# Optimization experiments

Measured on AMD Instinct MI355X. Metric: run time of the kernel, lower is better.

## Reference

```python
import jax, jax.numpy as jnp
import numpy as np

WIDTH = 2048
NUM_HEADS = 16
HEAD_DIM = WIDTH // NUM_HEADS  # 128
ROPE_DIMS = HEAD_DIM // 2      # 64, partial rotary
WINDOW = 512
ROPE_BASE = 10000.0
NEG_INF = -1e9


def apply_rope(x, dims, offset=0, base=ROPE_BASE):
    # x: [B, H, L, hd]; non-traditional (half-split) rotary on first `dims` dims.
    L = x.shape[2]
    half = dims // 2
    pos = (offset + jnp.arange(L)).astype(x.dtype)                     # [L]
    inv_freq = jnp.exp(-jnp.log(jnp.asarray(base, x.dtype)) * (jnp.arange(0, dims, 2).astype(x.dtype) / dims))  # [half]
    theta = pos[:, None] * inv_freq[None, :]                           # [L, half]
    cos = jnp.cos(theta)[None, None]                                   # [1,1,L,half]
    sin = jnp.sin(theta)[None, None]
    x1 = x[..., :half]
    x2 = x[..., half:dims]
    rest = x[..., dims:]
    rx1 = x1 * cos - x2 * sin
    rx2 = x1 * sin + x2 * cos
    return jnp.concatenate([rx1, rx2, rest], axis=-1)


def setup_inputs() -> dict:
    key = jax.random.key(0)
    ks = jax.random.split(key, 6)
    B, L, D, hd = 2, 2048, WIDTH, HEAD_DIM
    x = jax.random.normal(ks[0], (B, L, D), dtype=jnp.float32)
    Wq = jax.random.normal(ks[1], (D, D), dtype=jnp.float32) * 0.02
    Wk = jax.random.normal(ks[2], (D, hd), dtype=jnp.float32) * 0.02
    Wv = jax.random.normal(ks[3], (D, hd), dtype=jnp.float32) * 0.02
    Wo = jax.random.normal(ks[4], (D, D), dtype=jnp.float32) * 0.02
    bo = jax.random.normal(ks[5], (D,), dtype=jnp.float32) * 0.02
    return {"x": x, "Wq": Wq, "Wk": Wk, "Wv": Wv, "Wo": Wo, "bo": bo}


def reference(x, Wq, Wk, Wv, Wo, bo):
    B, L, D = x.shape
    H, hd = NUM_HEADS, HEAD_DIM
    scale = hd ** (-0.5)

    q = (x @ Wq).reshape(B, L, H, hd).transpose(0, 2, 1, 3)   # [B,H,L,hd]
    k = (x @ Wk).reshape(B, L, 1, hd).transpose(0, 2, 1, 3)   # [B,1,L,hd] (MQA)
    v = (x @ Wv).reshape(B, L, 1, hd).transpose(0, 2, 1, 3)

    q = apply_rope(q, ROPE_DIMS)
    k = apply_rope(k, ROPE_DIMS)

    # sliding-window causal mask: attend iff 0 <= i - j < WINDOW
    i = jnp.arange(L)[:, None]
    j = jnp.arange(L)[None, :]
    allowed = (i - j >= 0) & (i - j < WINDOW)                  # [L,L]
    mask = jnp.where(allowed, 0.0, NEG_INF).astype(x.dtype)

    scores = jnp.einsum("bhqd,bkd->bhqk", q, k[:, 0]) * scale  # [B,H,L,L]
    scores = scores + mask[None, None]
    attn = jax.nn.softmax(scores, axis=-1)
    out = jnp.einsum("bhqk,bkd->bhqd", attn, v[:, 0])          # [B,H,L,hd]
    out = out.transpose(0, 2, 1, 3).reshape(B, L, D)
    return out @ Wo + bo
```

## Files before the change

### kernel.cpp

```cpp
#include <hip/hip_runtime.h>
#include <hip/hip_bf16.h>
#include <stdint.h>


typedef float  f32x4  __attribute__((ext_vector_type(4)));
typedef __bf16 bf16x8 __attribute__((ext_vector_type(8)));

#define ASYNC_LD16(gp, lp)                                                     \
  __builtin_amdgcn_global_load_lds(                                            \
      (__attribute__((address_space(1))) void*)(gp),                           \
      (__attribute__((address_space(3))) void*)(lp), 16, 0, 0)

__global__ __launch_bounds__(256) void prep_all(
    const float* __restrict__ x, __hip_bfloat16* __restrict__ xb,
    const float* __restrict__ Wq, const float* __restrict__ Wk,
    const float* __restrict__ Wv, const float* __restrict__ Wo,
    __hip_bfloat16* __restrict__ wqkvT, __hip_bfloat16* __restrict__ woT) {
  __shared__ float t[32][33];
  int bid = blockIdx.x;
  if (bid < 8192) {
    const int i = bid * 256 + threadIdx.x;
    const float4 v = ((const float4*)x)[i];
    __align__(8) __hip_bfloat16 o[4] = {
        __float2bfloat16(v.x), __float2bfloat16(v.y),
        __float2bfloat16(v.z), __float2bfloat16(v.w)};
    *(uint2*)(xb + (size_t)i * 4) = *(uint2*)o;
    return;
  }
  bid -= 8192;
  const float* src;
  __hip_bfloat16* dst;
  int C, cb, rb;
  if (bid < 4096) {
    src = Wq; dst = wqkvT; C = 2048; cb = bid & 63; rb = bid >> 6;
  } else if (bid < 4352) {
    const int l = bid - 4096;
    src = Wk; dst = wqkvT + 2048ull * 2048; C = 128; cb = l & 3; rb = l >> 2;
  } else if (bid < 4608) {
    const int l = bid - 4352;
    src = Wv; dst = wqkvT + 2176ull * 2048; C = 128; cb = l & 3; rb = l >> 2;
  } else {
    const int l = bid - 4608;
    src = Wo; dst = woT; C = 2048; cb = l & 63; rb = l >> 6;
  }
  const int c0 = cb * 32, r0 = rb * 32;
  const int xx = threadIdx.x & 31, y = threadIdx.x >> 5;
#pragma unroll
  for (int i = 0; i < 32; i += 8)
    t[y + i][xx] = src[(size_t)(r0 + y + i) * C + c0 + xx];
  __syncthreads();
#pragma unroll
  for (int i = 0; i < 32; i += 8)
    dst[(size_t)(c0 + y + i) * 2048 + r0 + xx] = __float2bfloat16(t[xx][y + i]);
}

__device__ __forceinline__ void gemm_core64(const __bf16* __restrict__ A,
                                            const __bf16* __restrict__ BT,
                                            int K, __bf16* As, __bf16* Bs,
                                            f32x4 (&acc)[4][4]) {
  const int tid = threadIdx.x;
  const int wave = tid >> 6;
  const int lane = tid & 63;
  const int m0 = blockIdx.y * 128;
  const int n0 = blockIdx.x * 128;
  const int wm = (wave & 1) * 64;
  const int wn = (wave >> 1) * 64;
  const int ln = lane & 15;
  const int quad = lane >> 4;
  const int rdoff = (quad ^ ((ln >> 1) & 3)) * 8;

  size_t goff[4];
  int ldsoff[4];
#pragma unroll
  for (int i = 0; i < 4; i++) {
    const int cidx = (wave * 4 + i) * 64 + lane;
    const int p = cidx >> 9;
    const int pidx = cidx & 511;
    const int row = pidx >> 2;
    const int cc = pidx & 3;
    const int cg = cc ^ ((row >> 1) & 3);
    goff[i] = (size_t)row * K + p * 32 + cg * 8;
    ldsoff[i] = (wave * 4 + i) * 512;
  }
  const __bf16* Abase = A + (size_t)m0 * K;
  const __bf16* Bbase = BT + (size_t)n0 * K;

  for (int k0 = 0; k0 < K; k0 += 64) {
#pragma unroll
    for (int i = 0; i < 4; i++)
      ASYNC_LD16(Abase + k0 + goff[i], As + ldsoff[i]);
#pragma unroll
    for (int i = 0; i < 4; i++)
      ASYNC_LD16(Bbase + k0 + goff[i], Bs + ldsoff[i]);
    __syncthreads();
    bf16x8 af[4][2], bf[4][2];
#pragma unroll
    for (int i = 0; i < 4; i++)
#pragma unroll
      for (int p = 0; p < 2; p++)
        af[i][p] = *(const bf16x8*)&As[p * 4096 + (wm + i * 16 + ln) * 32 + rdoff];
#pragma unroll
    for (int j = 0; j < 4; j++)
#pragma unroll
      for (int p = 0; p < 2; p++)
        bf[j][p] = *(const bf16x8*)&Bs[p * 4096 + (wn + j * 16 + ln) * 32 + rdoff];
#pragma unroll
    for (int p = 0; p < 2; p++)
#pragma unroll
      for (int i = 0; i < 4; i++)
#pragma unroll
        for (int j = 0; j < 4; j++)
          acc[i][j] = __builtin_amdgcn_mfma_f32_16x16x32_bf16(af[i][p], bf[j][p],
                                                              acc[i][j], 0, 0, 0);
    __syncthreads();
  }
}

__global__ __launch_bounds__(256) void gemm_qkv(
    const __bf16* __restrict__ A, const __bf16* __restrict__ BT,
    __hip_bfloat16* __restrict__ qd, __hip_bfloat16* __restrict__ kd,
    __hip_bfloat16* __restrict__ vtd, int K) {
  __shared__ __align__(16) __bf16 As[128 * 64];
  __shared__ __align__(16) __bf16 Bs[128 * 64];
  f32x4 acc[4][4];
  const f32x4 zero = {0.f, 0.f, 0.f, 0.f};
#pragma unroll
  for (int i = 0; i < 4; i++)
#pragma unroll
    for (int j = 0; j < 4; j++) acc[i][j] = zero;
  gemm_core64(A, BT, K, As, Bs, acc);

  const int tid = threadIdx.x;
  const int wave = tid >> 6;
  const int lane = tid & 63;
  const int quad = lane >> 4;
  const int ln = lane & 15;
  const int m0 = blockIdx.y * 128;
  const int n0 = blockIdx.x * 128;
  const int wm = (wave & 1) * 64;
  const int wn = (wave >> 1) * 64;

  if (n0 == 2176) {
    const int bb = m0 >> 11;
    const int mloc = m0 & 2047;
#pragma unroll
    for (int i = 0; i < 4; i++) {
      const int rb = mloc + wm + i * 16 + quad * 4;
#pragma unroll
      for (int j = 0; j < 4; j++) {
        const int col = wn + j * 16 + ln;
        __align__(8) __hip_bfloat16 t4[4];
#pragma unroll
        for (int r = 0; r < 4; r++) t4[r] = __float2bfloat16(acc[i][j][r]);
        *(uint2*)(vtd + ((size_t)(bb * 128 + col)) * 2048 + rb) = *(uint2*)t4;
      }
    }
    return;
  }

  __hip_bfloat16* dst;
  int dstride, dcol;
  if (n0 < 2048) {
    dst = qd; dstride = 2048; dcol = n0;
  } else {
    dst = kd; dstride = 128; dcol = 0;
  }
  const bool dorope = (wn == 0);
  float invf0 = 0.f, invf1 = 0.f;
  if (dorope) {
    invf0 = expf(-0.28782313662425574f * (float)ln);
    invf1 = expf(-0.28782313662425574f * (float)(16 + ln));
  }

#pragma unroll
  for (int i = 0; i < 4; i++) {
#pragma unroll
    for (int r = 0; r < 4; r++) {
      const int row = m0 + wm + i * 16 + quad * 4 + r;
      float o0 = acc[i][0][r], o1 = acc[i][1][r];
      float o2 = acc[i][2][r], o3 = acc[i][3][r];
      if (dorope) {
        const float pos = (float)(row & 2047);
        float s0, c0, s1, c1;
        __sincosf(pos * invf0, &s0, &c0);
        __sincosf(pos * invf1, &s1, &c1);
        const float a0 = o0, b0 = o2, a1 = o1, b1 = o3;
        o0 = a0 * c0 - b0 * s0;
        o2 = a0 * s0 + b0 * c0;
        o1 = a1 * c1 - b1 * s1;
        o3 = a1 * s1 + b1 * c1;
      }
      __hip_bfloat16* rp = dst + (size_t)row * dstride + dcol + wn + ln;
      rp[0]  = __float2bfloat16(o0);
      rp[16] = __float2bfloat16(o1);
      rp[32] = __float2bfloat16(o2);
      rp[48] = __float2bfloat16(o3);
    }
  }
}

__global__ __launch_bounds__(256) void gemm_out(
    const __bf16* __restrict__ A, const __bf16* __restrict__ BT,
    float* __restrict__ C, const float* __restrict__ bias, int N, int K) {
  __shared__ __align__(16) __bf16 As[128 * 64];
  __shared__ __align__(16) __bf16 Bs[128 * 64];
  f32x4 acc[4][4];
  const f32x4 zero = {0.f, 0.f, 0.f, 0.f};
#pragma unroll
  for (int i = 0; i < 4; i++)
#pragma unroll
    for (int j = 0; j < 4; j++) acc[i][j] = zero;
  gemm_core64(A, BT, K, As, Bs, acc);

  const int tid = threadIdx.x;
  const int wave = tid >> 6;
  const int lane = tid & 63;
  const int m0 = blockIdx.y * 128;
  const int n0 = blockIdx.x * 128;
  const int wm = (wave & 1) * 64;
  const int wn = (wave >> 1) * 64;
  const int lrow = lane & 15;
#pragma unroll
  for (int j = 0; j < 4; j++) {
    const int col = n0 + wn + j * 16 + lrow;
    const float bv = bias[col];
#pragma unroll
    for (int i = 0; i < 4; i++) {
#pragma unroll
      for (int r = 0; r < 4; r++) {
        const int row = m0 + wm + i * 16 + (lane >> 4) * 4 + r;
        C[(size_t)row * N + col] = acc[i][j][r] + bv;
      }
    }
  }
}

__global__ __launch_bounds__(256) void attn_mfma(
    const __bf16* __restrict__ qb,
    const __bf16* __restrict__ kb,
    const __bf16* __restrict__ vtb,
    __hip_bfloat16* __restrict__ o)
{
  __shared__ __align__(16) __bf16 Ks[4][64 * 32];
  __shared__ __align__(16) __bf16 Vs[2][128 * 32];
  __shared__ __align__(16) __bf16 Ps[4][2][2][512];
  const int tid = threadIdx.x;
  const int wave = tid >> 6;
  const int lane = tid & 63;
  const int quad = lane >> 4;
  const int ln = lane & 15;
  const int bid = blockIdx.x;
  const int q0 = (bid & 15) * 128;
  const int h = (bid >> 4) & 15;
  const int b = bid >> 8;
  const int swr = (ln >> 1) & 3;
  const int rdoff = (quad ^ swr) * 8;

  bf16x8 qf[2][4];
#pragma unroll
  for (int g = 0; g < 2; g++) {
    const __bf16* qrow =
        qb + ((size_t)(b * 2048 + q0 + wave * 32 + g * 16 + ln)) * 2048 + h * 128;
#pragma unroll
    for (int ks = 0; ks < 4; ks++)
      qf[g][ks] = *(const bf16x8*)(qrow + ks * 32 + quad * 8);
  }

  f32x4 oacc[2][8];
  const f32x4 zero = {0.f, 0.f, 0.f, 0.f};
#pragma unroll
  for (int g = 0; g < 2; g++)
#pragma unroll
    for (int nb = 0; nb < 8; nb++) oacc[g][nb] = zero;
  float li[2][4] = {{0.f, 0.f, 0.f, 0.f}, {0.f, 0.f, 0.f, 0.f}};
  const float scale = 0.08838834764831845f;

  const __bf16* kbase = kb + (size_t)b * 2048 * 128;
  const __bf16* vbase = vtb + (size_t)b * 128 * 2048;

  const int tstart = (q0 >= 512) ? 0 : (512 - q0) / 64;
  for (int t = tstart; t < 10; ++t) {
    const int jt = q0 - 512 + 64 * t;
    __syncthreads();
    {
      const int key4 = lane >> 2, uu = lane & 3;
      const int sw = (key4 >> 1) & 3;
#pragma unroll
      for (int i = 0; i < 4; ++i) {
        const int c = wave * 4 + i;
        const int ks = c & 3, keybase = (c >> 2) * 16;
        ASYNC_LD16(kbase + (size_t)(jt + keybase + key4) * 128 + ks * 32 +
                       (uu ^ sw) * 8,
                   &Ks[ks][keybase * 32]);
      }
#pragma unroll
      for (int i = 0; i < 4; ++i) {
        const int c = wave * 4 + i;
        const int p = c & 1, dbase = (c >> 1) * 16;
        ASYNC_LD16(vbase + (size_t)(dbase + key4) * 2048 + jt + p * 32 +
                       (uu ^ sw) * 8,
                   &Vs[p][dbase * 32]);
      }
    }
    __syncthreads();

    f32x4 sacc[2][4];
#pragma unroll
    for (int g = 0; g < 2; g++)
#pragma unroll
      for (int j = 0; j < 4; j++) sacc[g][j] = zero;
#pragma unroll
    for (int j = 0; j < 4; j++)
#pragma unroll
      for (int ks = 0; ks < 4; ks++) {
        const bf16x8 kf = *(const bf16x8*)&Ks[ks][(j * 16 + ln) * 32 + rdoff];
#pragma unroll
        for (int g = 0; g < 2; g++)
          sacc[g][j] = __builtin_amdgcn_mfma_f32_16x16x32_bf16(qf[g][ks], kf,
                                                               sacc[g][j], 0, 0, 0);
      }

#pragma unroll
    for (int g = 0; g < 2; g++)
#pragma unroll
      for (int j = 0; j < 4; j++)
#pragma unroll
        for (int r = 0; r < 4; r++) {
          float v = sacc[g][j][r] * scale;
          const int d0 = (wave * 32 + g * 16 + quad * 4 + r) - (j * 16 + ln);
          if (t <= 1 && d0 >= (t << 6)) v = -1e30f;
          if (t >= 8 && d0 < ((t - 8) << 6)) v = -1e30f;
          v = fminf(v, 60.f);
          const float p = __expf(v);
          li[g][r] += p;
          const int ch = (j & 1) * 2 + (ln >> 3);
          const int swp = (quad * 2 + (r >> 1)) & 3;
          Ps[wave][g][j >> 1]
            [(quad * 4 + r) * 32 + (ch ^ swp) * 8 + (ln & 7)] = (__bf16)p;
        }

    const bf16x8 pf00 = *(const bf16x8*)&Ps[wave][0][0][ln * 32 + rdoff];
    const bf16x8 pf01 = *(const bf16x8*)&Ps[wave][0][1][ln * 32 + rdoff];
    const bf16x8 pf10 = *(const bf16x8*)&Ps[wave][1][0][ln * 32 + rdoff];
    const bf16x8 pf11 = *(const bf16x8*)&Ps[wave][1][1][ln * 32 + rdoff];
#pragma unroll
    for (int nb = 0; nb < 8; nb++) {
      const bf16x8 vf0 = *(const bf16x8*)&Vs[0][(nb * 16 + ln) * 32 + rdoff];
      const bf16x8 vf1 = *(const bf16x8*)&Vs[1][(nb * 16 + ln) * 32 + rdoff];
      oacc[0][nb] =
          __builtin_amdgcn_mfma_f32_16x16x32_bf16(pf00, vf0, oacc[0][nb], 0, 0, 0);
      oacc[0][nb] =
          __builtin_amdgcn_mfma_f32_16x16x32_bf16(pf01, vf1, oacc[0][nb], 0, 0, 0);
      oacc[1][nb] =
          __builtin_amdgcn_mfma_f32_16x16x32_bf16(pf10, vf0, oacc[1][nb], 0, 0, 0);
      oacc[1][nb] =
          __builtin_amdgcn_mfma_f32_16x16x32_bf16(pf11, vf1, oacc[1][nb], 0, 0, 0);
    }
  }

#pragma unroll
  for (int off = 1; off < 16; off <<= 1)
#pragma unroll
    for (int g = 0; g < 2; g++)
#pragma unroll
      for (int r = 0; r < 4; r++) li[g][r] += __shfl_xor(li[g][r], off);

#pragma unroll
  for (int g = 0; g < 2; g++) {
    __hip_bfloat16* obase =
        o + ((size_t)(b * 2048 + q0 + wave * 32 + g * 16 + quad * 4)) * 2048 +
        h * 128 + ln;
#pragma unroll
    for (int r = 0; r < 4; r++) {
      const float inv = 1.0f / li[g][r];
#pragma unroll
      for (int nb = 0; nb < 8; nb++)
        obase[(size_t)r * 2048 + nb * 16] = __float2bfloat16(oacc[g][nb][r] * inv);
    }
  }
}

extern "C" void kernel_launch(void* const* d_in, const int* in_sizes, int n_in,
                              void* d_out, int out_size, void* d_ws,
                              size_t ws_size, hipStream_t stream) {
  const float* x = (const float*)d_in[0];
  const float* Wq = (const float*)d_in[1];
  const float* Wk = (const float*)d_in[2];
  const float* Wv = (const float*)d_in[3];
  const float* Wo = (const float*)d_in[4];
  const float* bo = (const float*)d_in[5];
  float* out = (float*)d_out;

  char* w = (char*)d_ws;
  auto alloc = [&](size_t bytes) {
    void* p = (void*)w;
    w += (bytes + 255) & ~(size_t)255;
    return p;
  };
  __bf16* xb = (__bf16*)alloc(4096ull * 2048 * 2);
  __hip_bfloat16* wqkvT = (__hip_bfloat16*)alloc(2304ull * 2048 * 2);
  __hip_bfloat16* woT = (__hip_bfloat16*)alloc(2048ull * 2048 * 2);
  __hip_bfloat16* qbuf = (__hip_bfloat16*)alloc(4096ull * 2048 * 2);
  __hip_bfloat16* kbuf = (__hip_bfloat16*)alloc(4096ull * 128 * 2);
  __hip_bfloat16* vtb = (__hip_bfloat16*)alloc(4096ull * 128 * 2);
  __hip_bfloat16* attnb = (__hip_bfloat16*)xb;

  prep_all<<<16896, 256, 0, stream>>>(x, (__hip_bfloat16*)xb, Wq, Wk, Wv, Wo,
                                      wqkvT, woT);

  gemm_qkv<<<dim3(18, 32), 256, 0, stream>>>(xb, (const __bf16*)wqkvT, qbuf,
                                             kbuf, vtb, 2048);

  attn_mfma<<<512, 256, 0, stream>>>((const __bf16*)qbuf, (const __bf16*)kbuf,
                                     (const __bf16*)vtb, attnb);

  gemm_out<<<dim3(16, 32), 256, 0, stream>>>((const __bf16*)attnb,
                                             (const __bf16*)woT, out, bo, 2048,
                                             2048);
}
```

Measured before the change: 259.7 us.

## Double-buffer K/V tiles in attention and specialize mask modes via templates

The attention kernel now keeps two shared-memory K/V buffers. It issues the async global-to-LDS loads for the next tile before computing the current one, so each iteration needs one barrier instead of two and load latency can overlap MFMA work. The per-tile compute is moved into a templated helper, so the unmasked middle tiles skip the mask comparisons entirely. The cost is doubled LDS use for K/V, which may lower occupancy. The loop also relies on the trailing barrier and the async-load wait semantics being correct for the prefetched buffer.

Result: no change. 263.3 us (+1.4%).

```diff
diff --git a/kernel.cpp b/kernel.cpp
--- a/kernel.cpp
+++ b/kernel.cpp
@@ -235,15 +235,112 @@
   }
 }
 
+__device__ __forceinline__ void stage_kv(const __bf16* __restrict__ kbase,
+                                         const __bf16* __restrict__ vbase,
+                                         int jt, __bf16* Kb, __bf16* Vb,
+                                         int wave, int lane) {
+  const int key4 = lane >> 2, uu = lane & 3;
+  const int sw = (key4 >> 1) & 3;
+#pragma unroll
+  for (int i = 0; i < 4; ++i) {
+    const int c = wave * 4 + i;
+    const int ks = c & 3, keybase = (c >> 2) * 16;
+    ASYNC_LD16(kbase + (size_t)(jt + keybase + key4) * 128 + ks * 32 +
+                   (uu ^ sw) * 8,
+               Kb + ks * 2048 + keybase * 32);
+  }
+#pragma unroll
+  for (int i = 0; i < 4; ++i) {
+    const int c = wave * 4 + i;
+    const int p = c & 1, dbase = (c >> 1) * 16;
+    ASYNC_LD16(vbase + (size_t)(dbase + key4) * 2048 + jt + p * 32 +
+                   (uu ^ sw) * 8,
+               Vb + p * 4096 + dbase * 32);
+  }
+}
+
+template <int MODE>
+__device__ __forceinline__ void attn_tile(
+    const __bf16* __restrict__ Kb, const __bf16* __restrict__ Vb,
+    __bf16* __restrict__ PsW, const bf16x8 (&qf)[2][4], f32x4 (&oacc)[2][8],
+    float (&li)[2][4], int t, int wave, int quad, int ln, int rdoff) {
+  const f32x4 zero = {0.f, 0.f, 0.f, 0.f};
+  const float scale = 0.08838834764831845f;
+
+  f32x4 sacc[2][4];
+#pragma unroll
+  for (int g = 0; g < 2; g++)
+#pragma unroll
+    for (int j = 0; j < 4; j++) sacc[g][j] = zero;
+#pragma unroll
+  for (int j = 0; j < 4; j++)
+#pragma unroll
+    for (int ks = 0; ks < 4; ks++) {
+      const bf16x8 kf =
+          *(const bf16x8*)&Kb[ks * 2048 + (j * 16 + ln) * 32 + rdoff];
+#pragma unroll
+      for (int g = 0; g < 2; g++)
+        sacc[g][j] = __builtin_amdgcn_mfma_f32_16x16x32_bf16(qf[g][ks], kf,
+                                                             sacc[g][j], 0, 0, 0);
+    }
+
+#pragma unroll
+  for (int g = 0; g < 2; g++)
+#pragma unroll
+    for (int j = 0; j < 4; j++) {
+      const int ch = (j & 1) * 2 + (ln >> 3);
+#pragma unroll
+      for (int rp = 0; rp < 2; rp++) {
+        const int swp = (quad * 2 + rp) & 3;
+        __bf16* pw = PsW + (g * 2 + (j >> 1)) * 512 + (quad * 4 + rp * 2) * 32 +
+                     (ch ^ swp) * 8 + (ln & 7);
+#pragma unroll
+        for (int r2 = 0; r2 < 2; r2++) {
+          const int r = rp * 2 + r2;
+          float vv = sacc[g][j][r] * scale;
+          if (MODE == 1) {
+            const int d0 = (wave * 32 + g * 16 + quad * 4 + r) - (j * 16 + ln);
+            if (d0 >= (t << 6)) vv = -1e30f;
+          } else if (MODE == 2) {
+            const int d0 = (wave * 32 + g * 16 + quad * 4 + r) - (j * 16 + ln);
+            if (d0 < ((t - 8) << 6)) vv = -1e30f;
+          }
+          vv = fminf(vv, 60.f);
+          const float p = __expf(vv);
+          li[g][r] += p;
+          pw[r2 * 32] = (__bf16)p;
+        }
+      }
+    }
+
+  const bf16x8 pf00 = *(const bf16x8*)&PsW[0 * 512 + ln * 32 + rdoff];
+  const bf16x8 pf01 = *(const bf16x8*)&PsW[1 * 512 + ln * 32 + rdoff];
+  const bf16x8 pf10 = *(const bf16x8*)&PsW[2 * 512 + ln * 32 + rdoff];
+  const bf16x8 pf11 = *(const bf16x8*)&PsW[3 * 512 + ln * 32 + rdoff];
+#pragma unroll
+  for (int nb = 0; nb < 8; nb++) {
+    const bf16x8 vf0 = *(const bf16x8*)&Vb[(nb * 16 + ln) * 32 + rdoff];
+    const bf16x8 vf1 = *(const bf16x8*)&Vb[4096 + (nb * 16 + ln) * 32 + rdoff];
+    oacc[0][nb] =
+        __builtin_amdgcn_mfma_f32_16x16x32_bf16(pf00, vf0, oacc[0][nb], 0, 0, 0);
+    oacc[0][nb] =
+        __builtin_amdgcn_mfma_f32_16x16x32_bf16(pf01, vf1, oacc[0][nb], 0, 0, 0);
+    oacc[1][nb] =
+        __builtin_amdgcn_mfma_f32_16x16x32_bf16(pf10, vf0, oacc[1][nb], 0, 0, 0);
+    oacc[1][nb] =
+        __builtin_amdgcn_mfma_f32_16x16x32_bf16(pf11, vf1, oacc[1][nb], 0, 0, 0);
+  }
+}
+
 __global__ __launch_bounds__(256) void attn_mfma(
     const __bf16* __restrict__ qb,
     const __bf16* __restrict__ kb,
     const __bf16* __restrict__ vtb,
     __hip_bfloat16* __restrict__ o)
 {
-  __shared__ __align__(16) __bf16 Ks[4][64 * 32];
-  __shared__ __align__(16) __bf16 Vs[2][128 * 32];
-  __shared__ __align__(16) __bf16 Ps[4][2][2][512];
+  __shared__ __align__(16) __bf16 Ks[2][4 * 2048];
+  __shared__ __align__(16) __bf16 Vs[2][2 * 4096];
+  __shared__ __align__(16) __bf16 Ps[4][4 * 512];
   const int tid = threadIdx.x;
   const int wave = tid >> 6;
   const int lane = tid & 63;
@@ -253,8 +350,7 @@
   const int q0 = (bid & 15) * 128;
   const int h = (bid >> 4) & 15;
   const int b = bid >> 8;
-  const int swr = (ln >> 1) & 3;
-  const int rdoff = (quad ^ swr) * 8;
+  const int rdoff = (quad ^ ((ln >> 1) & 3)) * 8;
 
   bf16x8 qf[2][4];
 #pragma unroll
@@ -273,89 +369,27 @@
 #pragma unroll
     for (int nb = 0; nb < 8; nb++) oacc[g][nb] = zero;
   float li[2][4] = {{0.f, 0.f, 0.f, 0.f}, {0.f, 0.f, 0.f, 0.f}};
-  const float scale = 0.08838834764831845f;
 
   const __bf16* kbase = kb + (size_t)b * 2048 * 128;
   const __bf16* vbase = vtb + (size_t)b * 128 * 2048;
+  __bf16* PsW = Ps[wave];
 
   const int tstart = (q0 >= 512) ? 0 : (512 - q0) / 64;
+  stage_kv(kbase, vbase, q0 - 512 + 64 * tstart, Ks[0], Vs[0], wave, lane);
+  __syncthreads();
+
   for (int t = tstart; t < 10; ++t) {
-    const int jt = q0 - 512 + 64 * t;
+    const int cur = (t - tstart) & 1;
+    if (t + 1 < 10)
+      stage_kv(kbase, vbase, q0 - 512 + 64 * (t + 1), Ks[cur ^ 1], Vs[cur ^ 1],
+               wave, lane);
+    if (t <= 1)
+      attn_tile<1>(Ks[cur], Vs[cur], PsW, qf, oacc, li, t, wave, quad, ln, rdoff);
+    else if (t >= 8)
+      attn_tile<2>(Ks[cur], Vs[cur], PsW, qf, oacc, li, t, wave, quad, ln, rdoff);
+    else
+      attn_tile<0>(Ks[cur], Vs[cur], PsW, qf, oacc, li, t, wave, quad, ln, rdoff);
     __syncthreads();
-    {
-      const int key4 = lane >> 2, uu = lane & 3;
-      const int sw = (key4 >> 1) & 3;
-#pragma unroll
-      for (int i = 0; i < 4; ++i) {
-        const int c = wave * 4 + i;
-        const int ks = c & 3, keybase = (c >> 2) * 16;
-        ASYNC_LD16(kbase + (size_t)(jt + keybase + key4) * 128 + ks * 32 +
-                       (uu ^ sw) * 8,
-                   &Ks[ks][keybase * 32]);
-      }
-#pragma unroll
-      for (int i = 0; i < 4; ++i) {
-        const int c = wave * 4 + i;
-        const int p = c & 1, dbase = (c >> 1) * 16;
-        ASYNC_LD16(vbase + (size_t)(dbase + key4) * 2048 + jt + p * 32 +
-                       (uu ^ sw) * 8,
-                   &Vs[p][dbase * 32]);
-      }
-    }
-    __syncthreads();
-
-    f32x4 sacc[2][4];
-#pragma unroll
-    for (int g = 0; g < 2; g++)
-#pragma unroll
-      for (int j = 0; j < 4; j++) sacc[g][j] = zero;
-#pragma unroll
-    for (int j = 0; j < 4; j++)
-#pragma unroll
-      for (int ks = 0; ks < 4; ks++) {
-        const bf16x8 kf = *(const bf16x8*)&Ks[ks][(j * 16 + ln) * 32 + rdoff];
-#pragma unroll
-        for (int g = 0; g < 2; g++)
-          sacc[g][j] = __builtin_amdgcn_mfma_f32_16x16x32_bf16(qf[g][ks], kf,
-                                                               sacc[g][j], 0, 0, 0);
-      }
-
-#pragma unroll
-    for (int g = 0; g < 2; g++)
-#pragma unroll
-      for (int j = 0; j < 4; j++)
-#pragma unroll
-        for (int r = 0; r < 4; r++) {
-          float v = sacc[g][j][r] * scale;
-          const int d0 = (wave * 32 + g * 16 + quad * 4 + r) - (j * 16 + ln);
-          if (t <= 1 && d0 >= (t << 6)) v = -1e30f;
-          if (t >= 8 && d0 < ((t - 8) << 6)) v = -1e30f;
-          v = fminf(v, 60.f);
-          const float p = __expf(v);
-          li[g][r] += p;
-          const int ch = (j & 1) * 2 + (ln >> 3);
-          const int swp = (quad * 2 + (r >> 1)) & 3;
-          Ps[wave][g][j >> 1]
-            [(quad * 4 + r) * 32 + (ch ^ swp) * 8 + (ln & 7)] = (__bf16)p;
-        }
-
-    const bf16x8 pf00 = *(const bf16x8*)&Ps[wave][0][0][ln * 32 + rdoff];
-    const bf16x8 pf01 = *(const bf16x8*)&Ps[wave][0][1][ln * 32 + rdoff];
-    const bf16x8 pf10 = *(const bf16x8*)&Ps[wave][1][0][ln * 32 + rdoff];
-    const bf16x8 pf11 = *(const bf16x8*)&Ps[wave][1][1][ln * 32 + rdoff];
-#pragma unroll
-    for (int nb = 0; nb < 8; nb++) {
-      const bf16x8 vf0 = *(const bf16x8*)&Vs[0][(nb * 16 + ln) * 32 + rdoff];
-      const bf16x8 vf1 = *(const bf16x8*)&Vs[1][(nb * 16 + ln) * 32 + rdoff];
-      oacc[0][nb] =
-          __builtin_amdgcn_mfma_f32_16x16x32_bf16(pf00, vf0, oacc[0][nb], 0, 0, 0);
-      oacc[0][nb] =
-          __builtin_amdgcn_mfma_f32_16x16x32_bf16(pf01, vf1, oacc[0][nb], 0, 0, 0);
-      oacc[1][nb] =
-          __builtin_amdgcn_mfma_f32_16x16x32_bf16(pf10, vf0, oacc[1][nb], 0, 0, 0);
-      oacc[1][nb] =
-          __builtin_amdgcn_mfma_f32_16x16x32_bf16(pf11, vf1, oacc[1][nb], 0, 0, 0);
-    }
   }
 
 #pragma unroll
```
